# Kernel optimization log

Hardware: AMD Instinct MI355X
Metric: run time of the kernel (lower is better)

## Reference

```python
import jax, jax.numpy as jnp
import numpy as np
import math

H = 16
D_MODEL = 1024
D_K = 64
BS = 8
SEQ = 1024


def setup_inputs() -> dict:
    key = jax.random.key(0)
    ks = jax.random.split(key, 13)
    s = 1.0 / math.sqrt(D_MODEL)
    inp = {
        "q": jax.random.normal(ks[0], (BS, SEQ, D_MODEL), dtype=jnp.float32),
        "k": jax.random.normal(ks[1], (BS, SEQ, D_MODEL), dtype=jnp.float32),
        "v": jax.random.normal(ks[2], (BS, SEQ, D_MODEL), dtype=jnp.float32),
        "mask": jax.random.randint(ks[3], (BS, SEQ, SEQ), 0, 2, dtype=jnp.int32),
        "Wq": jax.random.normal(ks[4], (D_MODEL, D_MODEL), dtype=jnp.float32) * s,
        "bq": jax.random.normal(ks[5], (D_MODEL,), dtype=jnp.float32) * s,
        "Wk": jax.random.normal(ks[6], (D_MODEL, D_MODEL), dtype=jnp.float32) * s,
        "bk": jax.random.normal(ks[7], (D_MODEL,), dtype=jnp.float32) * s,
        "Wv": jax.random.normal(ks[8], (D_MODEL, D_MODEL), dtype=jnp.float32) * s,
        "bv": jax.random.normal(ks[9], (D_MODEL,), dtype=jnp.float32) * s,
        "Wo": jax.random.normal(ks[10], (D_MODEL, D_MODEL), dtype=jnp.float32) * s,
        "bo": jax.random.normal(ks[11], (D_MODEL,), dtype=jnp.float32) * s,
    }
    return inp


def reference(q, k, v, mask, Wq, bq, Wk, bk, Wv, bv, Wo, bo):
    bs, seq, _ = q.shape
    # projections, split heads: [b, h, s, dk]
    def proj(x, W, b):
        y = x @ W + b
        return y.reshape(bs, seq, H, D_K).transpose(0, 2, 1, 3)
    qh = proj(q, Wq, bq)
    kh = proj(k, Wk, bk)
    vh = proj(v, Wv, bv)
    # scaled dot-product attention (dropout is identity in eval mode)
    scores = jnp.einsum("bhqd,bhkd->bhqk", qh, kh) / math.sqrt(D_K)
    scores = jnp.where(mask[:, None, :, :] == 0, jnp.float32(-1e9), scores)
    attn = jax.nn.softmax(scores, axis=-1)
    ctx = jnp.einsum("bhqk,bhkd->bhqd", attn, vh)
    concat = ctx.transpose(0, 2, 1, 3).reshape(bs, seq, D_MODEL)
    return concat @ Wo + bo
```

## Files before the change

kernel.cpp:

```cpp
#include <hip/hip_runtime.h>
#include <hip/hip_bf16.h>

#define HN 16
#define DM 1024
#define DK 64
#define BSZ 8
#define SEQL 1024

typedef __attribute__((ext_vector_type(8))) short bf16x8;
typedef __attribute__((ext_vector_type(4))) short short4v;
typedef __attribute__((ext_vector_type(4))) float f32x4;

__device__ __forceinline__ short f2bf(float f) {
    union { float f; unsigned u; } x; x.f = f;
    unsigned u = x.u + 0x7FFFu + ((x.u >> 16) & 1u);
    return (short)(u >> 16);
}

__global__ __launch_bounds__(256) void transpose_cast(const float* __restrict__ W,
                                                      short* __restrict__ Wt) {
    __shared__ float tile[32][33];
    const int t = threadIdx.x;
    const int k0 = blockIdx.x * 32, n0 = blockIdx.y * 32;
    const int c = t & 31, r = t >> 5;
    #pragma unroll
    for (int p = 0; p < 4; ++p)
        tile[r + 8 * p][c] = W[(size_t)(k0 + r + 8 * p) * DM + n0 + c];
    __syncthreads();
    #pragma unroll
    for (int p = 0; p < 4; ++p)
        Wt[(size_t)(n0 + r + 8 * p) * DM + k0 + c] = f2bf(tile[c][r + 8 * p]);
}

__global__ __launch_bounds__(256) void pack_mask(const int* __restrict__ mask,
                                                 unsigned long long* __restrict__ bits) {
    size_t i = (size_t)blockIdx.x * 256 + threadIdx.x;
    unsigned long long b = __ballot(mask[i] != 0);
    if ((threadIdx.x & 63) == 0) bits[i >> 6] = b;
}

template <int MODE>
__global__ __launch_bounds__(256) void gemm_mfma(const void* __restrict__ Ap,
                                                 const short* __restrict__ Wt,
                                                 const float* __restrict__ bias,
                                                 void* __restrict__ Cp) {
    __shared__ __attribute__((aligned(16))) short As[128][40];
    __shared__ __attribute__((aligned(16))) short Bs[128][40];
    const int t = threadIdx.x;
    const int lane = t & 63, wv = t >> 6;
    const int wm = (wv >> 1) * 64, wn = (wv & 1) * 64;
    const int quad = lane >> 4, l15 = lane & 15;
    const int tileM = blockIdx.x * 128, tileN = blockIdx.y * 128;
    const size_t zoff = (size_t)blockIdx.z * DM * SEQL;

    f32x4 acc[4][4];
    #pragma unroll
    for (int i = 0; i < 4; ++i)
        #pragma unroll
        for (int j = 0; j < 4; ++j) acc[i][j] = {0.f, 0.f, 0.f, 0.f};

    for (int k0 = 0; k0 < DM; k0 += 32) {
        if (MODE != 1) {
            const float* A = (const float*)Ap + zoff;
            const int r0 = t >> 3, c4 = (t & 7) * 4;
            #pragma unroll
            for (int p = 0; p < 4; ++p) {
                int row = r0 + 32 * p;
                float4 v = *(const float4*)(A + (size_t)(tileM + row) * DM + k0 + c4);
                short4v s4 = {f2bf(v.x), f2bf(v.y), f2bf(v.z), f2bf(v.w)};
                *(short4v*)&As[row][c4] = s4;
            }
        } else {
            const short* A = (const short*)Ap + zoff;
            const int r0 = t >> 2, c8 = (t & 3) * 8;
            #pragma unroll
            for (int p = 0; p < 2; ++p) {
                int row = r0 + 64 * p;
                *(bf16x8*)&As[row][c8] =
                    *(const bf16x8*)(A + (size_t)(tileM + row) * DM + k0 + c8);
            }
        }
        {
            const int r0 = t >> 2, c8 = (t & 3) * 8;
            #pragma unroll
            for (int p = 0; p < 2; ++p) {
                int row = r0 + 64 * p;
                *(bf16x8*)&Bs[row][c8] =
                    *(const bf16x8*)(Wt + (size_t)(tileN + row) * DM + k0 + c8);
            }
        }
        __syncthreads();
        bf16x8 a[4], b[4];
        #pragma unroll
        for (int i = 0; i < 4; ++i) a[i] = *(const bf16x8*)&As[wm + i * 16 + l15][quad * 8];
        #pragma unroll
        for (int j = 0; j < 4; ++j) b[j] = *(const bf16x8*)&Bs[wn + j * 16 + l15][quad * 8];
        #pragma unroll
        for (int i = 0; i < 4; ++i)
            #pragma unroll
            for (int j = 0; j < 4; ++j)
                acc[i][j] = __builtin_amdgcn_mfma_f32_16x16x32_bf16(a[i], b[j], acc[i][j], 0, 0, 0);
        __syncthreads();
    }

    #pragma unroll
    for (int i = 0; i < 4; ++i)
        #pragma unroll
        for (int j = 0; j < 4; ++j)
            #pragma unroll
            for (int rr = 0; rr < 4; ++rr) {
                int row = tileM + wm + i * 16 + quad * 4 + rr;
                int col = tileN + wn + j * 16 + l15;
                float v = acc[i][j][rr] + bias[col];
                if (MODE == 0) {
                    short* C = (short*)Cp + zoff;
                    C[((size_t)(col >> 6) * SEQL + row) * DK + (col & 63)] = f2bf(v);
                } else if (MODE == 1) {
                    float* C = (float*)Cp + zoff;
                    C[(size_t)row * DM + col] = v;
                } else {
                    short* C = (short*)Cp + zoff;
                    C[(size_t)col * SEQL + row] = f2bf(v);
                }
            }
}

template <bool USE_BITS>
__global__ __launch_bounds__(256) void attn_mfma(const short* __restrict__ Qw,
                                                 const short* __restrict__ Kw,
                                                 const short* __restrict__ Vt,
                                                 const void* __restrict__ maskp,
                                                 short* __restrict__ ctx) {
    __shared__ __attribute__((aligned(16))) short Qs[64][72];
    __shared__ __attribute__((aligned(16))) short Ks[64][72];
    __shared__ __attribute__((aligned(16))) short Vs[64][72];
    __shared__ __attribute__((aligned(16))) short Ps[4][16][72];
    const int t = threadIdx.x;
    const int lane = t & 63, w = t >> 6;
    const int quad = lane >> 4, l15 = lane & 15;
    const int q0 = blockIdx.x * 64;
    const int h = blockIdx.y;
    const size_t zoff = (size_t)blockIdx.z * DM * SEQL;
    const short* Qb = Qw + zoff + (size_t)h * SEQL * DK;
    const short* Kb = Kw + zoff + (size_t)h * SEQL * DK;
    const short* Vb = Vt + zoff + (size_t)h * DK * SEQL;

    #pragma unroll
    for (int p = 0; p < 2; ++p) {
        int cc = t + 256 * p;
        int row = cc >> 3, off = (cc & 7) * 8;
        *(bf16x8*)&Qs[row][off] = *(const bf16x8*)(Qb + (size_t)(q0 + row) * DK + off);
    }

    f32x4 o[4];
    #pragma unroll
    for (int td = 0; td < 4; ++td) o[td] = {0.f, 0.f, 0.f, 0.f};
    float Lacc[4] = {0.f, 0.f, 0.f, 0.f};

    for (int j0 = 0; j0 < SEQL; j0 += 64) {
        #pragma unroll
        for (int p = 0; p < 2; ++p) {
            int cc = t + 256 * p;
            int row = cc >> 3, off = (cc & 7) * 8;
            *(bf16x8*)&Ks[row][off] = *(const bf16x8*)(Kb + (size_t)(j0 + row) * DK + off);
            *(bf16x8*)&Vs[row][off] = *(const bf16x8*)(Vb + (size_t)row * SEQL + j0 + off);
        }
        __syncthreads();

        unsigned long long mw[4];
        if (USE_BITS) {
            const unsigned long long* mb =
                (const unsigned long long*)maskp + (size_t)blockIdx.z * SEQL * 16;
            #pragma unroll
            for (int rr = 0; rr < 4; ++rr)
                mw[rr] = mb[(size_t)(q0 + w * 16 + quad * 4 + rr) * 16 + (j0 >> 6)];
        }

        #pragma unroll
        for (int tn = 0; tn < 4; ++tn) {
            f32x4 s = {0.f, 0.f, 0.f, 0.f};
            #pragma unroll
            for (int ks = 0; ks < 2; ++ks) {
                bf16x8 aq = *(const bf16x8*)&Qs[w * 16 + l15][ks * 32 + quad * 8];
                bf16x8 bk = *(const bf16x8*)&Ks[tn * 16 + l15][ks * 32 + quad * 8];
                s = __builtin_amdgcn_mfma_f32_16x16x32_bf16(aq, bk, s, 0, 0, 0);
            }
            #pragma unroll
            for (int rr = 0; rr < 4; ++rr) {
                bool keep;
                if (USE_BITS) {
                    keep = (mw[rr] >> (tn * 16 + l15)) & 1ull;
                } else {
                    const int* mb = (const int*)maskp + (size_t)blockIdx.z * SEQL * SEQL;
                    keep = mb[(size_t)(q0 + w * 16 + quad * 4 + rr) * SEQL + j0 + tn * 16 + l15] != 0;
                }
                float p = keep ? __expf(s[rr] * 0.125f) : 0.0f;
                Lacc[rr] += p;
                Ps[w][quad * 4 + rr][tn * 16 + l15] = f2bf(p);
            }
        }
        #pragma unroll
        for (int td = 0; td < 4; ++td)
            #pragma unroll
            for (int ks = 0; ks < 2; ++ks) {
                bf16x8 ap = *(const bf16x8*)&Ps[w][l15][ks * 32 + quad * 8];
                bf16x8 bv = *(const bf16x8*)&Vs[td * 16 + l15][ks * 32 + quad * 8];
                o[td] = __builtin_amdgcn_mfma_f32_16x16x32_bf16(ap, bv, o[td], 0, 0, 0);
            }
        __syncthreads();
    }

    #pragma unroll
    for (int rr = 0; rr < 4; ++rr) {
        float l = Lacc[rr];
        l += __shfl_xor(l, 1);
        l += __shfl_xor(l, 2);
        l += __shfl_xor(l, 4);
        l += __shfl_xor(l, 8);
        Lacc[rr] = 1.0f / l;
    }
    short* cb = ctx + zoff;
    #pragma unroll
    for (int td = 0; td < 4; ++td)
        #pragma unroll
        for (int rr = 0; rr < 4; ++rr) {
            int rq = q0 + w * 16 + quad * 4 + rr;
            int cd = h * 64 + td * 16 + l15;
            cb[(size_t)rq * DM + cd] = f2bf(o[td][rr] * Lacc[rr]);
        }
}

extern "C" void kernel_launch(void* const* d_in, const int* in_sizes, int n_in,
                              void* d_out, int out_size, void* d_ws, size_t ws_size,
                              hipStream_t stream) {
    const float* q  = (const float*)d_in[0];
    const float* k  = (const float*)d_in[1];
    const float* v  = (const float*)d_in[2];
    const int* mask = (const int*)d_in[3];
    const float* Wq = (const float*)d_in[4];
    const float* bq = (const float*)d_in[5];
    const float* Wk = (const float*)d_in[6];
    const float* bk = (const float*)d_in[7];
    const float* Wv = (const float*)d_in[8];
    const float* bv = (const float*)d_in[9];
    const float* Wo = (const float*)d_in[10];
    const float* bo = (const float*)d_in[11];
    float* out = (float*)d_out;

    const size_t MB = (size_t)1 << 20;
    const size_t MEL = (size_t)1024 * 1024;
    char* base = (char*)d_ws;

    short* Wqt = (short*)(base + 0 * 2 * MB);
    short* Wkt = (short*)(base + 1 * 2 * MB);
    short* Wvt = (short*)(base + 2 * 2 * MB);
    short* Wot = (short*)(base + 3 * 2 * MB);

    int zdim;
    bool use_bits;
    if      (ws_size >= 74 * MB) { zdim = 8; use_bits = true; }
    else if (ws_size >= 42 * MB) { zdim = 4; use_bits = true; }
    else if (ws_size >= 26 * MB) { zdim = 2; use_bits = true; }
    else if (ws_size >= 18 * MB) { zdim = 1; use_bits = true; }
    else                         { zdim = 1; use_bits = false; }

    unsigned long long* bits = (unsigned long long*)(base + 8 * MB);
    char* bufs = base + (use_bits ? 9 : 8) * MB;
    const size_t bufB = (size_t)zdim * 2 * MB;
    short* Qw  = (short*)(bufs);
    short* Kw  = (short*)(bufs + bufB);
    short* Vw  = (short*)(bufs + 2 * bufB);
    short* ctx = (short*)(bufs + 3 * bufB);

    transpose_cast<<<dim3(32, 32), 256, 0, stream>>>(Wq, Wqt);
    transpose_cast<<<dim3(32, 32), 256, 0, stream>>>(Wk, Wkt);
    transpose_cast<<<dim3(32, 32), 256, 0, stream>>>(Wv, Wvt);
    transpose_cast<<<dim3(32, 32), 256, 0, stream>>>(Wo, Wot);
    if (use_bits)
        pack_mask<<<(BSZ * SEQL * SEQL) / 256, 256, 0, stream>>>(mask, bits);

    const int iters = BSZ / zdim;
    for (int it = 0; it < iters; ++it) {
        const size_t boff = (size_t)it * zdim * MEL;
        const float* qb = q + boff;
        const float* kb = k + boff;
        const float* vb = v + boff;
        float* ob = out + boff;
        const void* mb = use_bits
            ? (const void*)(bits + (size_t)it * zdim * SEQL * 16)
            : (const void*)(mask + (size_t)it * zdim * SEQL * SEQL);

        gemm_mfma<0><<<dim3(8, 8, zdim), 256, 0, stream>>>(qb, Wqt, bq, Qw);
        gemm_mfma<0><<<dim3(8, 8, zdim), 256, 0, stream>>>(kb, Wkt, bk, Kw);
        gemm_mfma<2><<<dim3(8, 8, zdim), 256, 0, stream>>>(vb, Wvt, bv, Vw);

        if (use_bits)
            attn_mfma<true><<<dim3(16, 16, zdim), 256, 0, stream>>>(Qw, Kw, Vw, mb, ctx);
        else
            attn_mfma<false><<<dim3(16, 16, zdim), 256, 0, stream>>>(Qw, Kw, Vw, mb, ctx);

        gemm_mfma<1><<<dim3(8, 8, zdim), 256, 0, stream>>>(ctx, Wot, bo, ob);
    }
}
```

Before: 433.9 us.

## Pre-cast projection inputs to bf16 and stage GEMM tiles via direct-to-LDS loads

Adds a separate cast kernel that converts each fp32 activation input to bf16 in the ctx scratch buffer before its projection GEMM. Every GEMM then takes bf16 A only and loads both A and W tiles with global_load_lds directly into unpadded shared memory, with no register round-trip. This removes in-GEMM conversion work and VGPR staging, but adds three extra kernel launches and an extra fp32-read/bf16-write pass over the inputs. Dropping the LDS padding may cause bank conflicts on the fragment reads.

After: 408.7 us. 1.06x faster.

```diff
diff --git a/kernel.cpp b/kernel.cpp
--- a/kernel.cpp
+++ b/kernel.cpp
@@ -15,6 +15,22 @@
     union { float f; unsigned u; } x; x.f = f;
     unsigned u = x.u + 0x7FFFu + ((x.u >> 16) & 1u);
     return (short)(u >> 16);
+}
+
+__device__ __forceinline__ void async16(const short* g, short* ldsbase) {
+    __builtin_amdgcn_global_load_lds(
+        (const __attribute__((address_space(1))) unsigned int*)g,
+        (__attribute__((address_space(3))) unsigned int*)ldsbase, 16, 0, 0);
+}
+
+__global__ __launch_bounds__(256) void cast_bf16(const float* __restrict__ in,
+                                                 short* __restrict__ out) {
+    size_t i = (size_t)blockIdx.x * 256 + threadIdx.x;
+    float4 a = ((const float4*)in)[2 * i];
+    float4 b = ((const float4*)in)[2 * i + 1];
+    bf16x8 r = {f2bf(a.x), f2bf(a.y), f2bf(a.z), f2bf(a.w),
+                f2bf(b.x), f2bf(b.y), f2bf(b.z), f2bf(b.w)};
+    ((bf16x8*)out)[i] = r;
 }
 
 __global__ __launch_bounds__(256) void transpose_cast(const float* __restrict__ W,
@@ -40,18 +56,22 @@
 }
 
 template <int MODE>
-__global__ __launch_bounds__(256) void gemm_mfma(const void* __restrict__ Ap,
+__global__ __launch_bounds__(256) void gemm_mfma(const short* __restrict__ A,
                                                  const short* __restrict__ Wt,
                                                  const float* __restrict__ bias,
                                                  void* __restrict__ Cp) {
-    __shared__ __attribute__((aligned(16))) short As[128][40];
-    __shared__ __attribute__((aligned(16))) short Bs[128][40];
+    __shared__ __attribute__((aligned(16))) short As[128][32];
+    __shared__ __attribute__((aligned(16))) short Bs[128][32];
     const int t = threadIdx.x;
     const int lane = t & 63, wv = t >> 6;
     const int wm = (wv >> 1) * 64, wn = (wv & 1) * 64;
     const int quad = lane >> 4, l15 = lane & 15;
     const int tileM = blockIdx.x * 128, tileN = blockIdx.y * 128;
     const size_t zoff = (size_t)blockIdx.z * DM * SEQL;
+    const short* Az = A + zoff;
+
+    const int sr = wv * 16 + (lane >> 2);
+    const int sc = (lane & 3) * 8;
 
     f32x4 acc[4][4];
     #pragma unroll
@@ -60,34 +80,12 @@
         for (int j = 0; j < 4; ++j) acc[i][j] = {0.f, 0.f, 0.f, 0.f};
 
     for (int k0 = 0; k0 < DM; k0 += 32) {
-        if (MODE != 1) {
-            const float* A = (const float*)Ap + zoff;
-            const int r0 = t >> 3, c4 = (t & 7) * 4;
-            #pragma unroll
-            for (int p = 0; p < 4; ++p) {
-                int row = r0 + 32 * p;
-                float4 v = *(const float4*)(A + (size_t)(tileM + row) * DM + k0 + c4);
-                short4v s4 = {f2bf(v.x), f2bf(v.y), f2bf(v.z), f2bf(v.w)};
-                *(short4v*)&As[row][c4] = s4;
-            }
-        } else {
-            const short* A = (const short*)Ap + zoff;
-            const int r0 = t >> 2, c8 = (t & 3) * 8;
-            #pragma unroll
-            for (int p = 0; p < 2; ++p) {
-                int row = r0 + 64 * p;
-                *(bf16x8*)&As[row][c8] =
-                    *(const bf16x8*)(A + (size_t)(tileM + row) * DM + k0 + c8);
-            }
-        }
-        {
-            const int r0 = t >> 2, c8 = (t & 3) * 8;
-            #pragma unroll
-            for (int p = 0; p < 2; ++p) {
-                int row = r0 + 64 * p;
-                *(bf16x8*)&Bs[row][c8] =
-                    *(const bf16x8*)(Wt + (size_t)(tileN + row) * DM + k0 + c8);
-            }
+        #pragma unroll
+        for (int p = 0; p < 2; ++p) {
+            async16(Az + (size_t)(tileM + p * 64 + sr) * DM + k0 + sc,
+                    &As[p * 64 + wv * 16][0]);
+            async16(Wt + (size_t)(tileN + p * 64 + sr) * DM + k0 + sc,
+                    &Bs[p * 64 + wv * 16][0]);
         }
         __syncthreads();
         bf16x8 a[4], b[4];
@@ -290,9 +288,13 @@
             ? (const void*)(bits + (size_t)it * zdim * SEQL * 16)
             : (const void*)(mask + (size_t)it * zdim * SEQL * SEQL);
 
-        gemm_mfma<0><<<dim3(8, 8, zdim), 256, 0, stream>>>(qb, Wqt, bq, Qw);
-        gemm_mfma<0><<<dim3(8, 8, zdim), 256, 0, stream>>>(kb, Wkt, bk, Kw);
-        gemm_mfma<2><<<dim3(8, 8, zdim), 256, 0, stream>>>(vb, Wvt, bv, Vw);
+        const int castGrid = zdim * 512;
+        cast_bf16<<<castGrid, 256, 0, stream>>>(qb, ctx);
+        gemm_mfma<0><<<dim3(8, 8, zdim), 256, 0, stream>>>(ctx, Wqt, bq, Qw);
+        cast_bf16<<<castGrid, 256, 0, stream>>>(kb, ctx);
+        gemm_mfma<0><<<dim3(8, 8, zdim), 256, 0, stream>>>(ctx, Wkt, bk, Kw);
+        cast_bf16<<<castGrid, 256, 0, stream>>>(vb, ctx);
+        gemm_mfma<2><<<dim3(8, 8, zdim), 256, 0, stream>>>(ctx, Wvt, bv, Vw);
 
         if (use_bits)
             attn_mfma<true><<<dim3(16, 16, zdim), 256, 0, stream>>>(Qw, Kw, Vw, mb, ctx);
```
